# Performance work log

Measured on AMD Instinct MI355X. Metric: run time of the kernel, lower is better.

Reference implementation:

```python
import jax, jax.numpy as jnp
import numpy as np

D = 1024
H = 16

def setup_inputs() -> dict:
    key = jax.random.key(0)
    k1, k2, k3 = jax.random.split(key, 3)
    x = jax.random.normal(k1, (2, 2048, D), dtype=jnp.float32)
    # torch Linear weights: qkv (3d, d), proj (d, d); y = x @ W.T
    w_qkv = jax.random.normal(k2, (3 * D, D), dtype=jnp.float32) * (1.0 / np.sqrt(D))
    w_proj = jax.random.normal(k3, (D, D), dtype=jnp.float32) * (1.0 / np.sqrt(D))
    return {"x": x, "w_qkv": w_qkv, "w_proj": w_proj}

def reference(x, w_qkv, w_proj):
    B, T, C = x.shape
    hd = C // H  # head dim
    qkv = x @ w_qkv.T                     # [B,T,3C]
    q, k, v = jnp.split(qkv, 3, axis=-1)
    q = q.reshape(B, T, H, hd).transpose(0, 2, 1, 3)  # [B,H,T,hd]
    k = k.reshape(B, T, H, hd).transpose(0, 2, 1, 3)
    v = v.reshape(B, T, H, hd).transpose(0, 2, 1, 3)
    att = jnp.einsum('bhqd,bhkd->bhqk', q, k) * (hd ** -0.5)  # [B,H,T,T]
    mask = jnp.triu(jnp.ones((T, T), dtype=bool), 1)
    att = jnp.where(mask, jnp.float32(-1e9), att)
    att = jax.nn.softmax(att, axis=-1)
    y = jnp.einsum('bhqk,bhkd->bhqd', att, v)  # [B,H,T,hd]
    y = y.transpose(0, 2, 1, 3).reshape(B, T, C)
    return y @ w_proj.T
```

## Files before the change

### kernel.cpp

```cpp
#include <hip/hip_runtime.h>
#include <hip/hip_bf16.h>


typedef __bf16 bf16;
typedef __bf16 bf16x8 __attribute__((ext_vector_type(8)));
typedef float f32x4 __attribute__((ext_vector_type(4)));

__device__ __forceinline__ bf16 f2bf(float f) {
    unsigned u = __builtin_bit_cast(unsigned, f);
    u += 0x7fffu + ((u >> 16) & 1u);
    unsigned short h = (unsigned short)(u >> 16);
    return __builtin_bit_cast(bf16, h);
}
__device__ __forceinline__ bf16 trunc_bf(float f) {
    unsigned u = __builtin_bit_cast(unsigned, f);
    return __builtin_bit_cast(bf16, (unsigned short)(u >> 16));
}

__device__ __forceinline__ bf16x8 ld8f(const float* p) {
    f32x4 a = *(const f32x4*)p;
    f32x4 b = *(const f32x4*)(p + 4);
    bf16x8 r;
#pragma unroll
    for (int i = 0; i < 4; i++) { r[i] = f2bf(a[i]); r[i + 4] = f2bf(b[i]); }
    return r;
}

__device__ __forceinline__ void st_out(bf16* p, float v)  { *p = f2bf(v); }
__device__ __forceinline__ void st_out(float* p, float v) { *p = v; }

__device__ __forceinline__ void lds_fence() {
    asm volatile("s_waitcnt lgkmcnt(0)" ::: "memory");
}

__global__ __launch_bounds__(256) void cvt_bf16(const float* __restrict__ src,
                                                bf16* __restrict__ dst, int n) {
    int i = (blockIdx.x * 256 + threadIdx.x) * 8;
    if (i < n) *(bf16x8*)&dst[i] = ld8f(&src[i]);
}

__device__ __forceinline__ void glds16(const bf16* g, bf16* l) {
    __builtin_amdgcn_global_load_lds(
        (const __attribute__((address_space(1))) void*)g,
        (__attribute__((address_space(3))) void*)l, 16, 0, 0);
}

template <typename TC, int BN>
__global__ __launch_bounds__(256) void gemm_glds(const bf16* __restrict__ A, int lda, int aoff,
                                                 const bf16* __restrict__ W,
                                                 TC* __restrict__ C, int N, int K) {
    constexpr int NI = (BN == 128) ? 4 : 2;
    __shared__ bf16 sA[2][128 * 32];
    __shared__ bf16 sW[2][BN * 32];
    const int bm = blockIdx.x * 128, bn = blockIdx.y * BN;
    const int tid = threadIdx.x;
    const int wave = tid >> 6, lane = tid & 63;
    const int quad = lane >> 4, l16 = lane & 15;
    const int rbase = (BN == 128) ? (wave >> 1) * 64 : wave * 32;
    const int cbase = (BN == 128) ? (wave & 1) * 64 : 0;
    const int r16 = lane >> 2, cl = lane & 3;
    const int gch = cl ^ ((r16 >> 1) & 3);
    const int sl  = (l16 >> 1) & 3;

    auto stage = [&](int bufi, int k0) {
#pragma unroll
        for (int t = 0; t < 2; t++) {
            int row = wave * 32 + t * 16 + r16;
            glds16(&A[(size_t)(bm + row) * lda + aoff + k0 + gch * 8],
                   &sA[bufi][(wave * 32 + t * 16) * 32]);
        }
        if (BN == 128) {
#pragma unroll
            for (int t = 0; t < 2; t++) {
                int row = wave * 32 + t * 16 + r16;
                glds16(&W[(size_t)(bn + row) * K + k0 + gch * 8],
                       &sW[bufi][(wave * 32 + t * 16) * 32]);
            }
        } else {
            int row = wave * 16 + r16;
            glds16(&W[(size_t)(bn + row) * K + k0 + gch * 8], &sW[bufi][(wave * 16) * 32]);
        }
    };

    f32x4 acc[NI][4] = {};

    stage(0, 0);
    asm volatile("s_waitcnt vmcnt(0)" ::: "memory");
    __syncthreads();

    const int nsteps = K >> 5;
    for (int s = 0; s < nsteps; s++) {
        const int buf = s & 1;
        if (s + 1 < nsteps) stage(buf ^ 1, (s + 1) * 32);

        bf16x8 af[NI], bfr[4];
#pragma unroll
        for (int i = 0; i < NI; i++)
            af[i] = *(bf16x8*)&sA[buf][(rbase + i * 16 + l16) * 32 + (quad ^ sl) * 8];
#pragma unroll
        for (int j = 0; j < 4; j++)
            bfr[j] = *(bf16x8*)&sW[buf][(cbase + j * 16 + l16) * 32 + (quad ^ sl) * 8];
#pragma unroll
        for (int i = 0; i < NI; i++)
#pragma unroll
            for (int j = 0; j < 4; j++)
                acc[i][j] = __builtin_amdgcn_mfma_f32_16x16x32_bf16(
                    af[i], bfr[j], acc[i][j], 0, 0, 0);

        asm volatile("s_waitcnt vmcnt(0)" ::: "memory");
        __syncthreads();
    }

#pragma unroll
    for (int i = 0; i < NI; i++)
#pragma unroll
        for (int j = 0; j < 4; j++)
#pragma unroll
            for (int r = 0; r < 4; r++) {
                int row = bm + rbase + i * 16 + quad * 4 + r;
                int col = bn + cbase + j * 16 + l16;
                st_out(&C[(size_t)row * N + col], acc[i][j][r]);
            }
}

__global__ __launch_bounds__(256) void transpose_v(const bf16* __restrict__ qkv,
                                                   bf16* __restrict__ vt) {
    __shared__ bf16 s[64][72];
    const int tt = blockIdx.x;
    const int bh = blockIdx.y;
    const int b = bh >> 4, h = bh & 15;
    const int tid = threadIdx.x;

    for (int c = tid; c < 512; c += 256) {
        int t = c >> 3, dc = (c & 7) * 8;
        *(bf16x8*)&s[t][dc] =
            *(const bf16x8*)&qkv[((size_t)(b * 2048 + tt * 64 + t)) * 3072 + 2048 + h * 64 + dc];
    }
    __syncthreads();
    for (int c = tid; c < 512; c += 256) {
        int d = c >> 3, tc = (c & 7) * 8;
        bf16x8 o;
#pragma unroll
        for (int e = 0; e < 8; e++) o[e] = s[tc + e][d];
        *(bf16x8*)&vt[((size_t)bh * 64 + d) * 2048 + tt * 64 + tc] = o;
    }
}

__global__ __launch_bounds__(256, 2) void attn(bf16* __restrict__ qkv,
                                               const bf16* __restrict__ vt) {
    const int bh = blockIdx.x;
    const int y  = blockIdx.y;
    const int g  = (y < 8) ? (15 - y) : (y - 8);
    const int b = bh >> 4, h = bh & 15;
    const int tid  = threadIdx.x;
    const int wave = tid >> 6;
    const int lane = tid & 63;
    const int quad = lane >> 4, l16 = lane & 15;

    __shared__ bf16 sK[2][64 * 64];
    __shared__ bf16 sV[2][64 * 64];
    __shared__ bf16 sP[4][32 * 90];
    bf16* sPw = sP[wave];

    bf16* base = qkv + (size_t)b * 2048 * 3072;
    const bf16* vbh = vt + (size_t)bh * 64 * 2048;

    const int iq = g * 4 + wave;
    const int qb = iq * 32;
    const int kint = iq >> 1;
    const int ktmax = 2 * g + 1;
    const float SC = 0.125f * 1.44269504f;

    const int srow = lane >> 3;
    const int schk = (lane & 7) ^ srow;

    auto stage = [&](int bufi, int kt) {
#pragma unroll
        for (int u = 0; u < 2; u++) {
            int s = wave * 2 + u;
            glds16(&base[(size_t)(kt * 64 + s * 8 + srow) * 3072 + 1024 + h * 64 + schk * 8],
                   &sK[bufi][s * 512]);
            glds16(&vbh[(size_t)(s * 8 + srow) * 2048 + kt * 64 + schk * 8],
                   &sV[bufi][s * 512]);
        }
    };

    bf16x8 qa[2][2];
#pragma unroll
    for (int rt = 0; rt < 2; rt++)
#pragma unroll
        for (int c = 0; c < 2; c++)
            qa[rt][c] = *(const bf16x8*)&base[(size_t)(qb + rt * 16 + l16) * 3072 +
                                              h * 64 + c * 32 + quad * 8];

    f32x4 acc[2][4] = {};
    float lpart[2][4] = {};
    const int sw = l16 & 7;

    auto body = [&](int kt, bool tail, int bufi) {
        const bf16* K = sK[bufi];
        const bf16* V = sV[bufi];

        bf16x8 kb[4][2], vb[4][2];
#pragma unroll
        for (int j = 0; j < 4; j++)
#pragma unroll
            for (int c = 0; c < 2; c++)
                kb[j][c] = *(const bf16x8*)&K[(j * 16 + l16) * 64 + ((c * 4 + quad) ^ sw) * 8];
#pragma unroll
        for (int dt = 0; dt < 4; dt++)
#pragma unroll
            for (int c = 0; c < 2; c++)
                vb[dt][c] = *(const bf16x8*)&V[(dt * 16 + l16) * 64 + ((c * 4 + quad) ^ sw) * 8];

        f32x4 S[2][4] = {};
#pragma unroll
        for (int j = 0; j < 4; j++)
#pragma unroll
            for (int rt = 0; rt < 2; rt++) {
                S[rt][j] = __builtin_amdgcn_mfma_f32_16x16x32_bf16(qa[rt][0], kb[j][0], S[rt][j], 0, 0, 0);
                S[rt][j] = __builtin_amdgcn_mfma_f32_16x16x32_bf16(qa[rt][1], kb[j][1], S[rt][j], 0, 0, 0);
            }

#pragma unroll
        for (int rt = 0; rt < 2; rt++)
#pragma unroll
            for (int j = 0; j < 4; j++)
#pragma unroll
                for (int r = 0; r < 4; r++) {
                    float p = exp2f(S[rt][j][r] * SC - 8.0f);
                    if (tail) {
                        int kg = kt * 64 + j * 16 + l16;
                        int qg = qb + rt * 16 + quad * 4 + r;
                        p = (kg > qg) ? 0.0f : p;
                    }
                    lpart[rt][r] += p;
                    sPw[(rt * 16 + quad * 4 + r) * 90 + j * 16 + l16] = trunc_bf(p);
                }
        lds_fence();

        bf16x8 pa[2][2];
#pragma unroll
        for (int rt = 0; rt < 2; rt++) {
            pa[rt][0] = *(bf16x8*)&sPw[(rt * 16 + l16) * 90 + quad * 8];
            pa[rt][1] = *(bf16x8*)&sPw[(rt * 16 + l16) * 90 + 32 + quad * 8];
        }
#pragma unroll
        for (int dt = 0; dt < 4; dt++)
#pragma unroll
            for (int rt = 0; rt < 2; rt++) {
                acc[rt][dt] = __builtin_amdgcn_mfma_f32_16x16x32_bf16(pa[rt][0], vb[dt][0], acc[rt][dt], 0, 0, 0);
                acc[rt][dt] = __builtin_amdgcn_mfma_f32_16x16x32_bf16(pa[rt][1], vb[dt][1], acc[rt][dt], 0, 0, 0);
            }
        lds_fence();
    };

    stage(0, 0);
    asm volatile("s_waitcnt vmcnt(0)" ::: "memory");
    __syncthreads();
    int buf = 0;
    for (int kt = 0; kt <= ktmax; kt++) {
        if (kt + 1 <= ktmax) stage(buf ^ 1, kt + 1);
        if (kt <= kint) body(kt, kt == kint, buf);
        asm volatile("s_waitcnt vmcnt(0)" ::: "memory");
        __syncthreads();
        buf ^= 1;
    }

#pragma unroll
    for (int off = 1; off < 16; off <<= 1)
#pragma unroll
        for (int rt = 0; rt < 2; rt++)
#pragma unroll
            for (int r = 0; r < 4; r++)
                lpart[rt][r] += __shfl_xor(lpart[rt][r], off);

#pragma unroll
    for (int rt = 0; rt < 2; rt++)
#pragma unroll
        for (int r = 0; r < 4; r++) {
            float inv = 1.0f / lpart[rt][r];
            int row = qb + rt * 16 + quad * 4 + r;
#pragma unroll
            for (int dt = 0; dt < 4; dt++) {
                int col = h * 64 + dt * 16 + l16;
                base[(size_t)row * 3072 + 2048 + col] = f2bf(acc[rt][dt][r] * inv);
            }
        }
}

extern "C" void kernel_launch(void* const* d_in, const int* in_sizes, int n_in,
                              void* d_out, int out_size, void* d_ws, size_t ws_size,
                              hipStream_t stream) {
    (void)out_size; (void)ws_size;
    const float *x = (const float*)d_in[0], *w_qkv = (const float*)d_in[1],
                *w_proj = (const float*)d_in[2];
    for (int i = 0; i < n_in; i++) {
        if (in_sizes[i] == 4194304) x = (const float*)d_in[i];
        else if (in_sizes[i] == 3145728) w_qkv = (const float*)d_in[i];
        else if (in_sizes[i] == 1048576) w_proj = (const float*)d_in[i];
    }

    float* out = (float*)d_out;
    bf16* xb   = (bf16*)d_out;
    bf16* qkv  = (bf16*)d_ws;
    bf16* r2   = qkv + (size_t)4096 * 3072;
    bf16* wqb  = r2;
    bf16* vt   = r2;
    bf16* wpb  = r2;

    cvt_bf16<<<dim3(2048), dim3(256), 0, stream>>>(x, xb, 4096 * 1024);
    cvt_bf16<<<dim3(1536), dim3(256), 0, stream>>>(w_qkv, wqb, 3072 * 1024);
    gemm_glds<bf16, 128><<<dim3(32, 24), dim3(256), 0, stream>>>(
        xb, 1024, 0, wqb, qkv, 3072, 1024);
    transpose_v<<<dim3(32, 32), dim3(256), 0, stream>>>(qkv, vt);
    attn<<<dim3(32, 16), dim3(256), 0, stream>>>(qkv, vt);
    cvt_bf16<<<dim3(512), dim3(256), 0, stream>>>(w_proj, wpb, 1024 * 1024);
    gemm_glds<float, 128><<<dim3(32, 8), dim3(256), 0, stream>>>(
        qkv, 3072, 2048, wpb, out, 1024, 1024);
}
```

Measured before the change: 220.1 us.

## Compute transposed S so P stays in registers, removing LDS round-trip

Swaps the MFMA operand order so QK^T is produced transposed (keys along rows, queries along lanes). Each lane then holds the probabilities in the layout the PV MFMA needs as its B operand, so P is packed into bf16 registers directly instead of being written to and read back from shared memory. This removes the per-wave sP buffer, the LDS fences, and most of the row-sum shuffles. Output stores become 4-wide bf16 vectors. V fragments are now gathered as two half-vector LDS reads to match the transposed layout, which may add LDS instructions.

```diff
diff --git a/kernel.cpp b/kernel.cpp
--- a/kernel.cpp
+++ b/kernel.cpp
@@ -4,6 +4,7 @@
 
 typedef __bf16 bf16;
 typedef __bf16 bf16x8 __attribute__((ext_vector_type(8)));
+typedef __bf16 bf16x4 __attribute__((ext_vector_type(4)));
 typedef float f32x4 __attribute__((ext_vector_type(4)));
 
 __device__ __forceinline__ bf16 f2bf(float f) {
@@ -12,9 +13,11 @@
     unsigned short h = (unsigned short)(u >> 16);
     return __builtin_bit_cast(bf16, h);
 }
-__device__ __forceinline__ bf16 trunc_bf(float f) {
-    unsigned u = __builtin_bit_cast(unsigned, f);
-    return __builtin_bit_cast(bf16, (unsigned short)(u >> 16));
+
+__device__ __forceinline__ unsigned pack2(float a, float b) {
+    unsigned ua = __builtin_bit_cast(unsigned, a);
+    unsigned ub = __builtin_bit_cast(unsigned, b);
+    return (ua >> 16) | (ub & 0xFFFF0000u);
 }
 
 __device__ __forceinline__ bf16x8 ld8f(const float* p) {
@@ -28,10 +31,6 @@
 
 __device__ __forceinline__ void st_out(bf16* p, float v)  { *p = f2bf(v); }
 __device__ __forceinline__ void st_out(float* p, float v) { *p = v; }
-
-__device__ __forceinline__ void lds_fence() {
-    asm volatile("s_waitcnt lgkmcnt(0)" ::: "memory");
-}
 
 __global__ __launch_bounds__(256) void cvt_bf16(const float* __restrict__ src,
                                                 bf16* __restrict__ dst, int n) {
@@ -159,8 +158,6 @@
 
     __shared__ bf16 sK[2][64 * 64];
     __shared__ bf16 sV[2][64 * 64];
-    __shared__ bf16 sP[4][32 * 90];
-    bf16* sPw = sP[wave];
 
     bf16* base = qkv + (size_t)b * 2048 * 3072;
     const bf16* vbh = vt + (size_t)bh * 64 * 2048;
@@ -194,65 +191,77 @@
                                               h * 64 + c * 32 + quad * 8];
 
     f32x4 acc[2][4] = {};
-    float lpart[2][4] = {};
+    float lpart[2] = {0.0f, 0.0f};
     const int sw = l16 & 7;
 
     auto body = [&](int kt, bool tail, int bufi) {
         const bf16* K = sK[bufi];
         const bf16* V = sV[bufi];
 
-        bf16x8 kb[4][2], vb[4][2];
+        bf16x8 kb[4][2];
 #pragma unroll
         for (int j = 0; j < 4; j++)
 #pragma unroll
             for (int c = 0; c < 2; c++)
                 kb[j][c] = *(const bf16x8*)&K[(j * 16 + l16) * 64 + ((c * 4 + quad) ^ sw) * 8];
+
+        bf16x8 vb[4][2];
 #pragma unroll
         for (int dt = 0; dt < 4; dt++)
 #pragma unroll
-            for (int c = 0; c < 2; c++)
-                vb[dt][c] = *(const bf16x8*)&V[(dt * 16 + l16) * 64 + ((c * 4 + quad) ^ sw) * 8];
+            for (int c = 0; c < 2; c++) {
+                const bf16* vr = &V[(dt * 16 + l16) * 64];
+                union { bf16x4 h[2]; bf16x8 v; } u;
+                u.h[0] = *(const bf16x4*)&vr[((4 * c +     (quad >> 1)) ^ sw) * 8 + (quad & 1) * 4];
+                u.h[1] = *(const bf16x4*)&vr[((4 * c + 2 + (quad >> 1)) ^ sw) * 8 + (quad & 1) * 4];
+                vb[dt][c] = u.v;
+            }
 
         f32x4 S[2][4] = {};
 #pragma unroll
         for (int j = 0; j < 4; j++)
 #pragma unroll
             for (int rt = 0; rt < 2; rt++) {
-                S[rt][j] = __builtin_amdgcn_mfma_f32_16x16x32_bf16(qa[rt][0], kb[j][0], S[rt][j], 0, 0, 0);
-                S[rt][j] = __builtin_amdgcn_mfma_f32_16x16x32_bf16(qa[rt][1], kb[j][1], S[rt][j], 0, 0, 0);
-            }
+                S[rt][j] = __builtin_amdgcn_mfma_f32_16x16x32_bf16(kb[j][0], qa[rt][0], S[rt][j], 0, 0, 0);
+                S[rt][j] = __builtin_amdgcn_mfma_f32_16x16x32_bf16(kb[j][1], qa[rt][1], S[rt][j], 0, 0, 0);
+            }
+
+        unsigned pk[2][4][2];
+#pragma unroll
+        for (int rt = 0; rt < 2; rt++) {
+            const int qg = qb + rt * 16 + l16;
+#pragma unroll
+            for (int j = 0; j < 4; j++) {
+                float p[4];
+#pragma unroll
+                for (int r = 0; r < 4; r++) {
+                    float pv = exp2f(S[rt][j][r] * SC - 8.0f);
+                    if (tail) {
+                        int kg = kt * 64 + j * 16 + quad * 4 + r;
+                        pv = (kg > qg) ? 0.0f : pv;
+                    }
+                    p[r] = pv;
+                }
+                lpart[rt] += (p[0] + p[1]) + (p[2] + p[3]);
+                pk[rt][j][0] = pack2(p[0], p[1]);
+                pk[rt][j][1] = pack2(p[2], p[3]);
+            }
+        }
 
 #pragma unroll
         for (int rt = 0; rt < 2; rt++)
 #pragma unroll
-            for (int j = 0; j < 4; j++)
-#pragma unroll
-                for (int r = 0; r < 4; r++) {
-                    float p = exp2f(S[rt][j][r] * SC - 8.0f);
-                    if (tail) {
-                        int kg = kt * 64 + j * 16 + l16;
-                        int qg = qb + rt * 16 + quad * 4 + r;
-                        p = (kg > qg) ? 0.0f : p;
-                    }
-                    lpart[rt][r] += p;
-                    sPw[(rt * 16 + quad * 4 + r) * 90 + j * 16 + l16] = trunc_bf(p);
-                }
-        lds_fence();
-
-        bf16x8 pa[2][2];
-#pragma unroll
-        for (int rt = 0; rt < 2; rt++) {
-            pa[rt][0] = *(bf16x8*)&sPw[(rt * 16 + l16) * 90 + quad * 8];
-            pa[rt][1] = *(bf16x8*)&sPw[(rt * 16 + l16) * 90 + 32 + quad * 8];
-        }
-#pragma unroll
-        for (int dt = 0; dt < 4; dt++)
-#pragma unroll
-            for (int rt = 0; rt < 2; rt++) {
-                acc[rt][dt] = __builtin_amdgcn_mfma_f32_16x16x32_bf16(pa[rt][0], vb[dt][0], acc[rt][dt], 0, 0, 0);
-                acc[rt][dt] = __builtin_amdgcn_mfma_f32_16x16x32_bf16(pa[rt][1], vb[dt][1], acc[rt][dt], 0, 0, 0);
-            }
-        lds_fence();
+            for (int c = 0; c < 2; c++) {
+                union { unsigned u[4]; bf16x8 v; } pb;
+                pb.u[0] = pk[rt][2 * c][0];
+                pb.u[1] = pk[rt][2 * c][1];
+                pb.u[2] = pk[rt][2 * c + 1][0];
+                pb.u[3] = pk[rt][2 * c + 1][1];
+#pragma unroll
+                for (int dt = 0; dt < 4; dt++)
+                    acc[rt][dt] = __builtin_amdgcn_mfma_f32_16x16x32_bf16(
+                        vb[dt][c], pb.v, acc[rt][dt], 0, 0, 0);
+            }
     };
 
     stage(0, 0);
@@ -268,25 +277,23 @@
     }
 
 #pragma unroll
-    for (int off = 1; off < 16; off <<= 1)
-#pragma unroll
-        for (int rt = 0; rt < 2; rt++)
-#pragma unroll
-            for (int r = 0; r < 4; r++)
-                lpart[rt][r] += __shfl_xor(lpart[rt][r], off);
-
-#pragma unroll
-    for (int rt = 0; rt < 2; rt++)
-#pragma unroll
-        for (int r = 0; r < 4; r++) {
-            float inv = 1.0f / lpart[rt][r];
-            int row = qb + rt * 16 + quad * 4 + r;
-#pragma unroll
-            for (int dt = 0; dt < 4; dt++) {
-                int col = h * 64 + dt * 16 + l16;
-                base[(size_t)row * 3072 + 2048 + col] = f2bf(acc[rt][dt][r] * inv);
-            }
-        }
+    for (int rt = 0; rt < 2; rt++) {
+        lpart[rt] += __shfl_xor(lpart[rt], 16);
+        lpart[rt] += __shfl_xor(lpart[rt], 32);
+    }
+
+#pragma unroll
+    for (int rt = 0; rt < 2; rt++) {
+        float inv = 1.0f / lpart[rt];
+        int row = qb + rt * 16 + l16;
+#pragma unroll
+        for (int dt = 0; dt < 4; dt++) {
+            bf16x4 o;
+#pragma unroll
+            for (int r = 0; r < 4; r++) o[r] = f2bf(acc[rt][dt][r] * inv);
+            *(bf16x4*)&base[(size_t)row * 3072 + 2048 + h * 64 + dt * 16 + quad * 4] = o;
+        }
+    }
 }
 
 extern "C" void kernel_launch(void* const* d_in, const int* in_sizes, int n_in,
```

After: 202.1 us. 8.2% less time.
